# Optimization experiments

Measured on AMD Instinct MI355X. Metric: run time of the kernel, lower is better.

Reference implementation:

```python
import jax, jax.numpy as jnp
import numpy as np

D_MODEL = 1024
D_STATE = 16
D_CONV = 4
EXPAND = 2
D_INNER = D_MODEL * EXPAND
BATCH = 4
SEQLEN = 4096


def setup_inputs() -> dict:
    key = jax.random.key(0)
    ks = jax.random.split(key, 10)
    s = 1.0 / np.sqrt(D_MODEL)
    si = 1.0 / np.sqrt(D_INNER)
    return {
        "x": jax.random.normal(ks[0], (BATCH, SEQLEN, D_MODEL), jnp.float32),
        "x_proj_w": jax.random.normal(ks[1], (D_INNER, D_MODEL), jnp.float32) * s,
        "dt_proj_w": jax.random.normal(ks[2], (D_INNER, D_MODEL), jnp.float32) * s,
        "dt_proj_b": jax.random.normal(ks[3], (D_INNER,), jnp.float32) * 0.1,
        "A_log": jax.random.normal(ks[4], (D_INNER, D_STATE), jnp.float32),
        "D": jnp.ones((D_INNER,), jnp.float32),
        "B_proj_w": jax.random.normal(ks[5], (D_STATE, D_MODEL), jnp.float32) * s,
        "C_proj_w": jax.random.normal(ks[6], (D_STATE, D_MODEL), jnp.float32) * s,
        "conv_w": jax.random.normal(ks[7], (D_INNER, 1, D_CONV), jnp.float32) * 0.5,
        "conv_b": jax.random.normal(ks[8], (D_INNER,), jnp.float32) * 0.1,
        "out_proj_w": jax.random.normal(ks[9], (D_MODEL, D_INNER), jnp.float32) * si,
    }


def _selective_scan(xc, delta, A, B, C, D):
    # xc, delta: (b, L, d_inner); B, C: (b, L, d_state); A: (d_inner, d_state)
    batch, seqlen, d_inner = xc.shape
    d_state = A.shape[1]

    def step(h, inp):
        x_t, dt, B_t, C_t = inp  # (b,di), (b,di), (b,ds), (b,ds)
        A_disc = jnp.exp(dt[:, :, None] * A[None])           # (b, di, ds)
        h = A_disc * h + (dt[:, :, None] * B_t[:, None, :]) * x_t[:, :, None]
        y_t = jnp.einsum('bds,bs->bd', h, C_t) + D[None, :] * x_t
        return h, y_t

    h0 = jnp.zeros((batch, d_inner, d_state), xc.dtype)
    xs = (jnp.swapaxes(xc, 0, 1), jnp.swapaxes(delta, 0, 1),
          jnp.swapaxes(B, 0, 1), jnp.swapaxes(C, 0, 1))
    _, ys = jax.lax.scan(step, h0, xs)  # ys: (L, b, d_inner)
    return jnp.swapaxes(ys, 0, 1)


def reference(x, x_proj_w, dt_proj_w, dt_proj_b, A_log, D, B_proj_w, C_proj_w, conv_w, conv_b, out_proj_w):
    seqlen = x.shape[1]
    x_inner = x @ x_proj_w.T  # (b, L, d_inner)
    # causal depthwise conv1d: torch pads both sides by d_conv-1 then keeps first L,
    # equivalent to left-pad (d_conv-1, 0)
    xc = jax.lax.conv_general_dilated(
        jnp.swapaxes(x_inner, 1, 2), conv_w,
        window_strides=(1,), padding=[(D_CONV - 1, 0)],
        dimension_numbers=('NCH', 'OIH', 'NCH'),
        feature_group_count=D_INNER)
    xc = jnp.swapaxes(xc + conv_b[None, :, None], 1, 2)
    xc = jax.nn.silu(xc)
    B = x @ B_proj_w.T
    C = x @ C_proj_w.T
    delta = jax.nn.softplus(x @ dt_proj_w.T + dt_proj_b)
    A = -jnp.exp(A_log.astype(jnp.float32))
    y = _selective_scan(xc, delta, A, B, C, D)
    return y @ out_proj_w.T
```

## Files before the change

kernel.cpp:

```cpp
#include <hip/hip_runtime.h>
#include <hip/hip_bf16.h>
#include <math.h>

typedef __bf16 bf16;
typedef __bf16 bf16x2 __attribute__((ext_vector_type(2)));
typedef __bf16 bf16x8 __attribute__((ext_vector_type(8)));
typedef float f32x4 __attribute__((ext_vector_type(4)));

#define AS_G __attribute__((address_space(1)))
#define AS_L __attribute__((address_space(3)))

__device__ __forceinline__ void async_ld16(const void* g, void* l) {
  __builtin_amdgcn_global_load_lds((const AS_G void*)g, (AS_L void*)l, 16, 0, 0);
}
__device__ __forceinline__ float fexp2(float x) { return __builtin_amdgcn_exp2f(x); }

__global__ void detect_dtype(const void* __restrict__ Dones, int* __restrict__ flag) {
  if (threadIdx.x == 0 && blockIdx.x == 0) {
    *flag = (*(const unsigned int*)Dones == 0x3F803F80u) ? 0 : 1;
  }
}

__global__ __launch_bounds__(256) void to_bf16(
    const void* __restrict__ src, bf16* __restrict__ dst, int n8,
    const int* __restrict__ flag)
{
  const int i = blockIdx.x * 256 + threadIdx.x;
  if (i >= n8) return;
  bf16x8 o;
  if (*flag) {
    const f32x4* s = (const f32x4*)src;
    f32x4 a = s[2*i], b = s[2*i + 1];
    #pragma unroll
    for (int e = 0; e < 4; ++e) { o[e] = (bf16)a[e]; o[e+4] = (bf16)b[e]; }
  } else {
    o = ((const bf16x8*)src)[i];
  }
  ((bf16x8*)dst)[i] = o;
}

template<int EPI>
__global__ __launch_bounds__(256, 2) void gemm_bt(
    const bf16* __restrict__ A, const bf16* __restrict__ W,
    bf16* __restrict__ OutB, float* __restrict__ OutF,
    const bf16* __restrict__ bias, const int* __restrict__ flag,
    int M, int N, int K)
{
  __shared__ bf16 smA[128*32];
  __shared__ bf16 smB[128*32];
  const int tid  = threadIdx.x;
  const int wave = tid >> 6;
  const int lane = tid & 63;
  const int m0 = blockIdx.x * 128;
  const int n0 = blockIdx.y * 128;
  const int wm = (wave >> 1) * 64;
  const int wn = (wave & 1) * 64;
  const int lm = lane & 15;
  const int q  = lane >> 4;
  const bool f32o = (EPI == 2) && (*flag != 0);

  f32x4 acc[4][4] = {};

  const int chunk0 = wave*128 + lane;
  const int chunk1 = wave*128 + 64 + lane;
  const int r0 = chunk0 >> 2, c0 = chunk0 & 3;
  const int r1 = chunk1 >> 2, c1 = chunk1 & 3;
  const bf16* gA0 = A + (size_t)(m0 + r0)*K + c0*8;
  const bf16* gA1 = A + (size_t)(m0 + r1)*K + c1*8;
  const bf16* gB0 = W + (size_t)(n0 + r0)*K + c0*8;
  const bf16* gB1 = W + (size_t)(n0 + r1)*K + c1*8;
  bf16* lA0 = smA + (size_t)(wave*128     )*8;
  bf16* lA1 = smA + (size_t)(wave*128 + 64)*8;
  bf16* lB0 = smB + (size_t)(wave*128     )*8;
  bf16* lB1 = smB + (size_t)(wave*128 + 64)*8;

  for (int k0 = 0; k0 < K; k0 += 32) {
    __syncthreads();
    async_ld16(gA0 + k0, lA0);
    async_ld16(gA1 + k0, lA1);
    async_ld16(gB0 + k0, lB0);
    async_ld16(gB1 + k0, lB1);
    __syncthreads();
    bf16x8 af[4], bfr[4];
    #pragma unroll
    for (int mi = 0; mi < 4; ++mi)
      af[mi] = *(const bf16x8*)(smA + (wm + mi*16 + lm)*32 + q*8);
    #pragma unroll
    for (int ni = 0; ni < 4; ++ni)
      bfr[ni] = *(const bf16x8*)(smB + (wn + ni*16 + lm)*32 + q*8);
    #pragma unroll
    for (int mi = 0; mi < 4; ++mi)
      #pragma unroll
      for (int ni = 0; ni < 4; ++ni)
        acc[mi][ni] = __builtin_amdgcn_mfma_f32_16x16x32_bf16(af[mi], bfr[ni], acc[mi][ni], 0, 0, 0);
  }

  #pragma unroll
  for (int mi = 0; mi < 4; ++mi) {
    #pragma unroll
    for (int ni = 0; ni < 4; ++ni) {
      const int col = n0 + wn + ni*16 + lm;
      float bval = 0.f;
      if (EPI == 1) bval = (float)bias[col];
      #pragma unroll
      for (int r = 0; r < 4; ++r) {
        const int row = m0 + wm + mi*16 + q*4 + r;
        float v = acc[mi][ni][r];
        if (EPI == 1) {
          v += bval;
          v = (v > 20.f) ? v : log1pf(__expf(v));
        }
        const size_t idx = (size_t)row*N + col;
        if (EPI == 2 && f32o) OutF[idx] = v;
        else                  OutB[idx] = (bf16)v;
      }
    }
  }
}

__global__ __launch_bounds__(64) void bc_gemm(
    const bf16* __restrict__ X,
    const bf16* __restrict__ Bw, const bf16* __restrict__ Cw,
    float* __restrict__ Bout, float* __restrict__ Cout)
{
  const int lane = threadIdx.x;
  const int lm = lane & 15, q = lane >> 4;
  const int m0 = blockIdx.x * 16;
  const bf16* W = blockIdx.y ? Cw : Bw;
  float* O      = blockIdx.y ? Cout : Bout;
  f32x4 acc = {};
  const bf16* pa = X + (size_t)(m0 + lm)*1024 + q*8;
  const bf16* pw = W + (size_t)lm*1024 + q*8;
  for (int k0 = 0; k0 < 1024; k0 += 32) {
    bf16x8 a = *(const bf16x8*)(pa + k0);
    bf16x8 w = *(const bf16x8*)(pw + k0);
    acc = __builtin_amdgcn_mfma_f32_16x16x32_bf16(a, w, acc, 0, 0, 0);
  }
  #pragma unroll
  for (int r = 0; r < 4; ++r)
    O[(size_t)(m0 + q*4 + r)*16 + lm] = acc[r];
}

__global__ __launch_bounds__(256) void conv_silu(
    const bf16* __restrict__ Xin, const bf16* __restrict__ cw,
    const bf16* __restrict__ cb, bf16* __restrict__ Xc)
{
  const int idx = blockIdx.x * 256 + threadIdx.x;
  const int row = idx >> 8;
  const int dv  = (idx & 255) * 8;
  const int t   = row & 4095;
  bf16x8 wv[4];
  const bf16x8* pw = (const bf16x8*)(cw + (size_t)dv*4);
  #pragma unroll
  for (int j = 0; j < 4; ++j) wv[j] = pw[j];
  bf16x8 bv = *(const bf16x8*)(cb + dv);
  float acc[8];
  #pragma unroll
  for (int e = 0; e < 8; ++e) acc[e] = (float)bv[e];
  #pragma unroll
  for (int j = 0; j < 4; ++j) {
    const int tr = t - 3 + j;
    if (tr < 0) continue;
    bf16x8 xv = *(const bf16x8*)(Xin + (size_t)(row - 3 + j)*2048 + dv);
    #pragma unroll
    for (int e = 0; e < 8; ++e) {
      const int li = e*4 + j;
      acc[e] += (float)xv[e] * (float)wv[li >> 3][li & 7];
    }
  }
  bf16x8 o;
  #pragma unroll
  for (int e = 0; e < 8; ++e) {
    float v = acc[e];
    v = v / (1.f + __expf(-v));
    o[e] = (bf16)v;
  }
  *(bf16x8*)(Xc + (size_t)row*2048 + dv) = o;
}

__global__ __launch_bounds__(256) void scan_phase1(
    const bf16* __restrict__ Xc, const bf16* __restrict__ Dt,
    const float* __restrict__ Bm, const bf16* __restrict__ A_log,
    float* __restrict__ Hend, float* __restrict__ Dtsum)
{
  const int tid = threadIdx.x;
  const int d0 = blockIdx.x * 512 + tid * 2;
  const int c = blockIdx.y;
  const int b = blockIdx.z;
  const int t0 = c * 128;
  __shared__ float sB[128*16];
  {
    const f32x4* src = (const f32x4*)(Bm + ((size_t)b*4096 + t0)*16);
    f32x4* dst = (f32x4*)sB;
    dst[tid]       = src[tid];
    dst[tid + 256] = src[tid + 256];
  }
  __syncthreads();
  float A2[2][16];
  #pragma unroll
  for (int u = 0; u < 2; ++u)
    #pragma unroll
    for (int s = 0; s < 16; ++s)
      A2[u][s] = -__expf((float)A_log[(d0+u)*16 + s]) * 1.44269504088896f;
  float h[2][16] = {};
  float dts[2] = {0.f, 0.f};
  const bf16* pX = Xc + ((size_t)b*4096 + t0)*2048 + d0;
  const bf16* pD = Dt + ((size_t)b*4096 + t0)*2048 + d0;
  bf16x2 vD = *(const bf16x2*)pD;
  bf16x2 vX = *(const bf16x2*)pX;
  for (int t = 0; t < 128; ++t) {
    bf16x2 nD = vD, nX = vX;
    if (t < 127) {
      nD = *(const bf16x2*)(pD + (size_t)(t+1)*2048);
      nX = *(const bf16x2*)(pX + (size_t)(t+1)*2048);
    }
    f32x4 Bv[4];
    #pragma unroll
    for (int i = 0; i < 4; ++i) Bv[i] = ((const f32x4*)(sB + t*16))[i];
    #pragma unroll
    for (int u = 0; u < 2; ++u) {
      const float dt = (float)vD[u];
      const float xv = (float)vX[u];
      dts[u] += dt;
      const float dx = dt * xv;
      #pragma unroll
      for (int s = 0; s < 16; ++s) {
        const float ad = fexp2(dt * A2[u][s]);
        h[u][s] = ad*h[u][s] + dx * Bv[s>>2][s&3];
      }
    }
    vD = nD; vX = nX;
  }
  #pragma unroll
  for (int u = 0; u < 2; ++u) {
    const size_t base = (((size_t)b*32 + c)*2048 + d0 + u)*16;
    #pragma unroll
    for (int s = 0; s < 16; ++s) Hend[base + s] = h[u][s];
    Dtsum[((size_t)b*32 + c)*2048 + d0 + u] = dts[u];
  }
}

__global__ __launch_bounds__(256) void scan_phase2(
    float* __restrict__ H,
    const float* __restrict__ Dtsum,
    const bf16* __restrict__ A_log)
{
  const int idx = blockIdx.x*256 + threadIdx.x;
  const int s = idx & 15;
  const int d = (idx >> 4) & 2047;
  const int b = idx >> 15;
  const float A2 = -__expf((float)A_log[d*16 + s]) * 1.44269504088896f;
  float h = 0.f;
  for (int c = 0; c < 32; ++c) {
    const size_t off = (((size_t)b*32 + c)*2048 + d)*16 + s;
    const float hend = H[off];
    H[off] = h;
    const float ap = fexp2(A2 * Dtsum[((size_t)b*32 + c)*2048 + d]);
    h = h*ap + hend;
  }
}

__global__ __launch_bounds__(256) void scan_phase3(
    const bf16* __restrict__ Xc, const bf16* __restrict__ Dt,
    const float* __restrict__ Bm, const float* __restrict__ Cm,
    const bf16* __restrict__ A_log, const bf16* __restrict__ Dvec,
    const float* __restrict__ Hstart, bf16* __restrict__ Y)
{
  const int tid = threadIdx.x;
  const int d0 = blockIdx.x * 512 + tid * 2;
  const int c = blockIdx.y;
  const int b = blockIdx.z;
  const int t0 = c * 128;
  __shared__ float sB[128*16];
  __shared__ float sC[128*16];
  {
    const f32x4* srcB = (const f32x4*)(Bm + ((size_t)b*4096 + t0)*16);
    const f32x4* srcC = (const f32x4*)(Cm + ((size_t)b*4096 + t0)*16);
    ((f32x4*)sB)[tid]       = srcB[tid];
    ((f32x4*)sB)[tid + 256] = srcB[tid + 256];
    ((f32x4*)sC)[tid]       = srcC[tid];
    ((f32x4*)sC)[tid + 256] = srcC[tid + 256];
  }
  __syncthreads();
  float A2[2][16];
  #pragma unroll
  for (int u = 0; u < 2; ++u)
    #pragma unroll
    for (int s = 0; s < 16; ++s)
      A2[u][s] = -__expf((float)A_log[(d0+u)*16 + s]) * 1.44269504088896f;
  float h[2][16];
  #pragma unroll
  for (int u = 0; u < 2; ++u) {
    const size_t base = (((size_t)b*32 + c)*2048 + d0 + u)*16;
    #pragma unroll
    for (int s = 0; s < 16; ++s) h[u][s] = Hstart[base + s];
  }
  const float Dd0 = (float)Dvec[d0];
  const float Dd1 = (float)Dvec[d0 + 1];
  const bf16* pX = Xc + ((size_t)b*4096 + t0)*2048 + d0;
  const bf16* pD = Dt + ((size_t)b*4096 + t0)*2048 + d0;
  bf16*       pY = Y  + ((size_t)b*4096 + t0)*2048 + d0;
  bf16x2 vD = *(const bf16x2*)pD;
  bf16x2 vX = *(const bf16x2*)pX;
  for (int t = 0; t < 128; ++t) {
    bf16x2 nD = vD, nX = vX;
    if (t < 127) {
      nD = *(const bf16x2*)(pD + (size_t)(t+1)*2048);
      nX = *(const bf16x2*)(pX + (size_t)(t+1)*2048);
    }
    f32x4 Bv[4], Cv[4];
    #pragma unroll
    for (int i = 0; i < 4; ++i) {
      Bv[i] = ((const f32x4*)(sB + t*16))[i];
      Cv[i] = ((const f32x4*)(sC + t*16))[i];
    }
    float y[2];
    #pragma unroll
    for (int u = 0; u < 2; ++u) {
      const float dt = (float)vD[u];
      const float xv = (float)vX[u];
      const float dx = dt * xv;
      y[u] = (u ? Dd1 : Dd0) * xv;
      #pragma unroll
      for (int s = 0; s < 16; ++s) {
        const float ad = fexp2(dt * A2[u][s]);
        h[u][s] = ad*h[u][s] + dx * Bv[s>>2][s&3];
        y[u] += h[u][s] * Cv[s>>2][s&3];
      }
    }
    bf16x2 yo; yo[0] = (bf16)y[0]; yo[1] = (bf16)y[1];
    *(bf16x2*)(pY + (size_t)t*2048) = yo;
    vD = nD; vX = nX;
  }
}

extern "C" void kernel_launch(void* const* d_in, const int* in_sizes, int n_in,
                              void* d_out, int out_size, void* d_ws, size_t ws_size,
                              hipStream_t stream)
{
  char* ws = (char*)d_ws;
  size_t off = 0;
  auto alloc = [&](size_t bytes) -> char* {
    char* p = ws + off; off += (bytes + 255) & ~(size_t)255; return p;
  };
  bf16*  xin = (bf16*) alloc((size_t)16384*2048*2);
  bf16*  dlt = (bf16*) alloc((size_t)16384*2048*2);
  bf16*  xc  = (bf16*) alloc((size_t)16384*2048*2);
  float* Bm  = (float*)alloc((size_t)16384*16*4);
  float* Cm  = (float*)alloc((size_t)16384*16*4);
  float* Hst = (float*)alloc((size_t)4*32*2048*16*4);
  float* Dts = (float*)alloc((size_t)4*32*2048*4);
  int*   flag = (int*) alloc(256);
  const int ncanon = 11;
  static const int canon_n[11] = {
    4*4096*1024, 2048*1024, 2048*1024, 2048, 2048*16, 2048,
    16*1024, 16*1024, 2048*4, 2048, 1024*2048 };
  bf16* canon[11];
  for (int i = 0; i < ncanon; ++i) canon[i] = (bf16*)alloc((size_t)canon_n[i]*2);
  if (off > ws_size) return;

  detect_dtype<<<1, 64, 0, stream>>>(d_in[5], flag);
  for (int i = 0; i < ncanon; ++i) {
    const int n8 = canon_n[i] / 8;
    to_bf16<<<(n8 + 255)/256, 256, 0, stream>>>(d_in[i], canon[i], n8, flag);
  }
  const bf16* x          = canon[0];
  const bf16* x_proj_w   = canon[1];
  const bf16* dt_proj_w  = canon[2];
  const bf16* dt_proj_b  = canon[3];
  const bf16* A_log      = canon[4];
  const bf16* Dvec       = canon[5];
  const bf16* B_proj_w   = canon[6];
  const bf16* C_proj_w   = canon[7];
  const bf16* conv_w     = canon[8];
  const bf16* conv_b     = canon[9];
  const bf16* out_proj_w = canon[10];

  gemm_bt<0><<<dim3(128,16), 256, 0, stream>>>(x, x_proj_w,  xin, nullptr, nullptr,   flag, 16384, 2048, 1024);
  gemm_bt<1><<<dim3(128,16), 256, 0, stream>>>(x, dt_proj_w, dlt, nullptr, dt_proj_b, flag, 16384, 2048, 1024);
  bc_gemm<<<dim3(1024,2), 64, 0, stream>>>(x, B_proj_w, C_proj_w, Bm, Cm);
  conv_silu<<<dim3(16384), 256, 0, stream>>>(xin, conv_w, conv_b, xc);
  scan_phase1<<<dim3(4,32,4), 256, 0, stream>>>(xc, dlt, Bm, A_log, Hst, Dts);
  scan_phase2<<<dim3(512),    256, 0, stream>>>(Hst, Dts, A_log);
  scan_phase3<<<dim3(4,32,4), 256, 0, stream>>>(xc, dlt, Bm, Cm, A_log, Dvec, Hst, xin );
  gemm_bt<2><<<dim3(128,8), 256, 0, stream>>>(xin, out_proj_w, (bf16*)d_out, (float*)d_out, nullptr, flag, 16384, 1024, 2048);
}
```

Before: 735.5 us.

## Double-buffer GEMM LDS tiles, swizzle LDS columns, use fast softplus log

```diff
diff --git a/kernel.cpp b/kernel.cpp
--- a/kernel.cpp
+++ b/kernel.cpp
@@ -46,8 +46,8 @@
     const bf16* __restrict__ bias, const int* __restrict__ flag,
     int M, int N, int K)
 {
-  __shared__ bf16 smA[128*32];
-  __shared__ bf16 smB[128*32];
+  __shared__ bf16 smA[2][128*32];
+  __shared__ bf16 smB[2][128*32];
   const int tid  = threadIdx.x;
   const int wave = tid >> 6;
   const int lane = tid & 63;
@@ -62,37 +62,52 @@
   f32x4 acc[4][4] = {};
 
   const int chunk0 = wave*128 + lane;
-  const int chunk1 = wave*128 + 64 + lane;
+  const int chunk1 = chunk0 + 64;
   const int r0 = chunk0 >> 2, c0 = chunk0 & 3;
   const int r1 = chunk1 >> 2, c1 = chunk1 & 3;
-  const bf16* gA0 = A + (size_t)(m0 + r0)*K + c0*8;
-  const bf16* gA1 = A + (size_t)(m0 + r1)*K + c1*8;
-  const bf16* gB0 = W + (size_t)(n0 + r0)*K + c0*8;
-  const bf16* gB1 = W + (size_t)(n0 + r1)*K + c1*8;
-  bf16* lA0 = smA + (size_t)(wave*128     )*8;
-  bf16* lA1 = smA + (size_t)(wave*128 + 64)*8;
-  bf16* lB0 = smB + (size_t)(wave*128     )*8;
-  bf16* lB1 = smB + (size_t)(wave*128 + 64)*8;
-
-  for (int k0 = 0; k0 < K; k0 += 32) {
-    __syncthreads();
-    async_ld16(gA0 + k0, lA0);
-    async_ld16(gA1 + k0, lA1);
-    async_ld16(gB0 + k0, lB0);
-    async_ld16(gB1 + k0, lB1);
-    __syncthreads();
+  const int sc0 = c0 ^ ((r0 >> 1) & 3);
+  const int sc1 = c1 ^ ((r1 >> 1) & 3);
+  const bf16* gA0 = A + (size_t)(m0 + r0)*K + sc0*8;
+  const bf16* gA1 = A + (size_t)(m0 + r1)*K + sc1*8;
+  const bf16* gB0 = W + (size_t)(n0 + r0)*K + sc0*8;
+  const bf16* gB1 = W + (size_t)(n0 + r1)*K + sc1*8;
+  const int oA0 = (wave*128     )*8;
+  const int oA1 = (wave*128 + 64)*8;
+
+  auto stage = [&](int buf, int k0) {
+    async_ld16(gA0 + k0, &smA[buf][oA0]);
+    async_ld16(gA1 + k0, &smA[buf][oA1]);
+    async_ld16(gB0 + k0, &smB[buf][oA0]);
+    async_ld16(gB1 + k0, &smB[buf][oA1]);
+  };
+
+  const int sl = (q ^ ((lm >> 1) & 3)) * 8;
+
+  auto compute = [&](const bf16* sA, const bf16* sB) {
     bf16x8 af[4], bfr[4];
     #pragma unroll
     for (int mi = 0; mi < 4; ++mi)
-      af[mi] = *(const bf16x8*)(smA + (wm + mi*16 + lm)*32 + q*8);
+      af[mi] = *(const bf16x8*)(sA + (wm + mi*16 + lm)*32 + sl);
     #pragma unroll
     for (int ni = 0; ni < 4; ++ni)
-      bfr[ni] = *(const bf16x8*)(smB + (wn + ni*16 + lm)*32 + q*8);
+      bfr[ni] = *(const bf16x8*)(sB + (wn + ni*16 + lm)*32 + sl);
     #pragma unroll
     for (int mi = 0; mi < 4; ++mi)
       #pragma unroll
       for (int ni = 0; ni < 4; ++ni)
         acc[mi][ni] = __builtin_amdgcn_mfma_f32_16x16x32_bf16(af[mi], bfr[ni], acc[mi][ni], 0, 0, 0);
+  };
+
+  stage(0, 0);
+  __syncthreads();
+
+  for (int k0 = 0; k0 < K; k0 += 64) {
+    stage(1, k0 + 32);
+    compute(smA[0], smB[0]);
+    __syncthreads();
+    if (k0 + 64 < K) stage(0, k0 + 64);
+    compute(smA[1], smB[1]);
+    __syncthreads();
   }
 
   #pragma unroll
@@ -108,7 +123,7 @@
         float v = acc[mi][ni][r];
         if (EPI == 1) {
           v += bval;
-          v = (v > 20.f) ? v : log1pf(__expf(v));
+          v = (v > 20.f) ? v : __logf(1.f + __expf(v));
         }
         const size_t idx = (size_t)row*N + col;
         if (EPI == 2 && f32o) OutF[idx] = v;
```

Result: faster. 661.6 us (-10.1%).
